# Kernel optimization log

Hardware: AMD Instinct MI355X
Metric: run time of the kernel (lower is better)

## Reference

```python
import jax, jax.numpy as jnp
import numpy as np

B_SZ, L_SEQ, D_MODEL, D_STATE = 4, 2048, 1024, 16


def setup_inputs() -> dict:
    key = jax.random.key(0)
    ks = jax.random.split(key, 6)
    x = jax.random.normal(ks[0], (B_SZ, L_SEQ, D_MODEL), jnp.float32)
    # HiPPO-inspired init: A_log = log(arange(1..n)).clamp(min=-7), broadcast over channels
    A_log = jnp.clip(jnp.log(jnp.arange(1, D_STATE + 1, dtype=jnp.float32)), -7.0, None)
    A_log = jnp.broadcast_to(A_log[None, :], (D_MODEL, D_STATE)).astype(jnp.float32)
    B_param = 0.02 * jax.random.normal(ks[1], (D_MODEL, D_STATE), jnp.float32)
    C_param = 0.02 * jax.random.normal(ks[2], (D_MODEL, D_STATE), jnp.float32)
    log_dt = 0.01 * jax.random.normal(ks[3], (D_MODEL,), jnp.float32) - 4.0
    in_w = jax.random.normal(ks[4], (2 * D_MODEL, D_MODEL), jnp.float32) / np.sqrt(D_MODEL).astype(np.float32)
    in_b = jnp.zeros((2 * D_MODEL,), jnp.float32)
    out_w = jax.random.normal(ks[5], (D_MODEL, D_MODEL), jnp.float32) / np.sqrt(D_MODEL).astype(np.float32)
    out_b = jnp.zeros((D_MODEL,), jnp.float32)
    ln_g = jnp.ones((D_MODEL,), jnp.float32)
    ln_b = jnp.zeros((D_MODEL,), jnp.float32)
    return {"x": x, "A_log": A_log, "B_param": B_param, "C_param": C_param,
            "log_dt": log_dt, "in_w": in_w, "in_b": in_b, "out_w": out_w,
            "out_b": out_b, "ln_g": ln_g, "ln_b": ln_b}


def _ssm_scan(u, A_log, B_param, C_param, log_dt):
    # u: (B, L, D). Builds kernel h[t,d] = sum_n A_bar[d,n]^t * C[d,n]*B[d,n]*dt[d]
    # and applies a causal depthwise convolution (via FFT; same math as conv1d).
    L = u.shape[1]
    dt = jnp.clip(jnp.exp(log_dt), 1e-4, 1.0)                      # (D,)
    A_bar = jnp.exp(-jnp.exp(A_log) * dt[:, None])                 # ZOH discretisation (D,N)
    A_bar = jnp.clip(A_bar, 1e-8, 1.0 - 1e-8)
    log_A = jnp.log(A_bar)                                         # (D,N)
    t_idx = jnp.arange(L, dtype=jnp.float32)                       # (L,)
    A_powers = jnp.exp(t_idx[:, None, None] * log_A[None, :, :])   # (L,D,N)
    cb_dt = C_param * B_param * dt[:, None]                        # (D,N)
    kernel = jnp.einsum('ldn,dn->ld', A_powers, cb_dt)             # (L,D)
    # causal conv: y[b,t,d] = sum_{tau<=t} kernel[tau,d] * u[b,t-tau,d]
    n_fft = 2 * L
    Kf = jnp.fft.rfft(kernel, n=n_fft, axis=0)                     # (n_fft/2+1, D)
    Uf = jnp.fft.rfft(u, n=n_fft, axis=1)                          # (B, n_fft/2+1, D)
    y = jnp.fft.irfft(Uf * Kf[None], n=n_fft, axis=1)[:, :L]       # (B,L,D)
    return y.astype(u.dtype)


def reference(x, A_log, B_param, C_param, log_dt, in_w, in_b, out_w, out_b, ln_g, ln_b):
    x = x.astype(jnp.float32)
    residual = x
    # LayerNorm (eps=1e-5)
    mu = jnp.mean(x, axis=-1, keepdims=True)
    var = jnp.mean(jnp.square(x - mu), axis=-1, keepdims=True)
    xn = (x - mu) * jax.lax.rsqrt(var + 1e-5) * ln_g + ln_b
    xz = xn @ in_w.T + in_b                                        # (B,L,2D)
    x_proj, z = xz[..., :D_MODEL], xz[..., D_MODEL:]
    z = jax.nn.silu(z)
    y = _ssm_scan(x_proj, A_log, B_param, C_param, log_dt)
    y = y * z
    y = y @ out_w.T + out_b
    # dropout is identity in eval mode
    return jnp.clip(y + residual, -10.0, 10.0)
```

## Files before the change

kernel.cpp:

```cpp
#include <hip/hip_runtime.h>
#include <hip/hip_bf16.h>

#define D_MODEL 1024
#define D_STATE 16
#define L_SEQ 2048
#define B_SZ 4
#define M_ROWS (B_SZ * L_SEQ)
#define N_CHUNK 32
#define C_LEN 64

typedef __attribute__((ext_vector_type(8))) short short8;
typedef __attribute__((ext_vector_type(4))) float f32x4;
typedef unsigned int u32;
typedef __attribute__((ext_vector_type(4))) u32 u32x4;

#define BAR() asm volatile("s_waitcnt lgkmcnt(0)\n\ts_barrier" ::: "memory")

static __device__ __forceinline__ unsigned short f2bf(float f) {
    unsigned int u = __float_as_uint(f);
    unsigned int r = (u + 0x7FFFu + ((u >> 16) & 1u)) >> 16;
    return (unsigned short)r;
}
static __device__ __forceinline__ float bf2f(unsigned short u) {
    return __uint_as_float(((unsigned int)u) << 16);
}

__global__ void conv_bf16_kernel(const float* __restrict__ src,
                                 unsigned short* __restrict__ dst, int n4) {
    int i = blockIdx.x * blockDim.x + threadIdx.x;
    if (i < n4) {
        float4 v = ((const float4*)src)[i];
        ushort4 o;
        o.x = f2bf(v.x); o.y = f2bf(v.y); o.z = f2bf(v.z); o.w = f2bf(v.w);
        ((ushort4*)dst)[i] = o;
    }
}

__global__ __launch_bounds__(256) void ln_kernel(const float* __restrict__ x,
                                                 const float* __restrict__ g,
                                                 const float* __restrict__ b,
                                                 unsigned short* __restrict__ xn) {
    int row = blockIdx.x;
    int t = threadIdx.x;
    const float4* xr = (const float4*)(x + (size_t)row * D_MODEL);
    float4 v = xr[t];
    float s  = v.x + v.y + v.z + v.w;
    float ss = v.x * v.x + v.y * v.y + v.z * v.z + v.w * v.w;
    #pragma unroll
    for (int o = 32; o > 0; o >>= 1) {
        s  += __shfl_down(s,  o);
        ss += __shfl_down(ss, o);
    }
    __shared__ float sbuf[8];
    int wid = t >> 6;
    if ((t & 63) == 0) { sbuf[wid] = s; sbuf[4 + wid] = ss; }
    __syncthreads();
    float S  = sbuf[0] + sbuf[1] + sbuf[2] + sbuf[3];
    float SS = sbuf[4] + sbuf[5] + sbuf[6] + sbuf[7];
    float mu  = S * (1.0f / D_MODEL);
    float var = SS * (1.0f / D_MODEL) - mu * mu;
    float inv = rsqrtf(var + 1e-5f);
    float4 gv = ((const float4*)g)[t];
    float4 bv = ((const float4*)b)[t];
    ushort4 o;
    o.x = f2bf((v.x - mu) * inv * gv.x + bv.x);
    o.y = f2bf((v.y - mu) * inv * gv.y + bv.y);
    o.z = f2bf((v.z - mu) * inv * gv.z + bv.z);
    o.w = f2bf((v.w - mu) * inv * gv.w + bv.w);
    ((ushort4*)(xn + (size_t)row * D_MODEL))[t] = o;
}

__global__ __launch_bounds__(256, 2) void gemm1_kernel(const unsigned short* __restrict__ A,
                                                       const unsigned short* __restrict__ Bt,
                                                       const float* __restrict__ bias,
                                                       unsigned short* __restrict__ u_bf,
                                                       unsigned short* __restrict__ zs) {
    __shared__ unsigned short lA[2][128 * 32];
    __shared__ unsigned short lB[2][256 * 32];
    const int K = D_MODEL;

    int t = threadIdx.x;
    int lane = t & 63;
    int wave = t >> 6;
    int wm = wave >> 1, wn = wave & 1;
    int m0 = blockIdx.x * 128;
    int n0 = blockIdx.y * 256;
    int row = lane & 15;
    int quad = lane >> 4;

    int sr = t >> 2;
    int sc = ((t & 3) ^ ((t >> 3) & 3)) * 8;
    const unsigned short* gA0 = A + (size_t)(m0 + sr) * K + sc;
    const unsigned short* gA1 = A + (size_t)(m0 + 64 + sr) * K + sc;
    const unsigned short* gB0 = Bt + (size_t)(n0 + sr) * K + sc;
    const unsigned short* gB1 = Bt + (size_t)(n0 + 64 + sr) * K + sc;
    const unsigned short* gB2 = Bt + (size_t)(n0 + 128 + sr) * K + sc;
    const unsigned short* gB3 = Bt + (size_t)(n0 + 192 + sr) * K + sc;

    int offA[4], offB[8];
    #pragma unroll
    for (int i = 0; i < 4; i++) {
        int r6 = i * 16 + row;
        int slot = r6 * 4 + (quad ^ ((r6 >> 1) & 3));
        offA[i] = wm * 2048 + slot * 8;
    }
    #pragma unroll
    for (int j = 0; j < 8; j++) {
        int r8 = wn * 128 + j * 16 + row;
        int half = r8 >> 6, r6 = r8 & 63;
        int slot = r6 * 4 + (quad ^ ((r6 >> 1) & 3));
        offB[j] = half * 2048 + slot * 8;
    }

    f32x4 acc[4][8] = {};

    u32x4 PA[6], PB[6];
    PA[0] = *(const u32x4*)gA0;        PA[1] = *(const u32x4*)gA1;
    PA[2] = *(const u32x4*)gB0;        PA[3] = *(const u32x4*)gB1;
    PA[4] = *(const u32x4*)gB2;        PA[5] = *(const u32x4*)gB3;
    PB[0] = *(const u32x4*)(gA0 + 32); PB[1] = *(const u32x4*)(gA1 + 32);
    PB[2] = *(const u32x4*)(gB0 + 32); PB[3] = *(const u32x4*)(gB1 + 32);
    PB[4] = *(const u32x4*)(gB2 + 32); PB[5] = *(const u32x4*)(gB3 + 32);

    for (int kk = 0; kk < K; kk += 64) {
        *(u32x4*)&lA[0][t * 8]        = PA[0];
        *(u32x4*)&lA[0][2048 + t * 8] = PA[1];
        *(u32x4*)&lB[0][t * 8]        = PA[2];
        *(u32x4*)&lB[0][2048 + t * 8] = PA[3];
        *(u32x4*)&lB[0][4096 + t * 8] = PA[4];
        *(u32x4*)&lB[0][6144 + t * 8] = PA[5];
        if (kk + 64 < K) {
            int kn = kk + 64;
            PA[0] = *(const u32x4*)(gA0 + kn); PA[1] = *(const u32x4*)(gA1 + kn);
            PA[2] = *(const u32x4*)(gB0 + kn); PA[3] = *(const u32x4*)(gB1 + kn);
            PA[4] = *(const u32x4*)(gB2 + kn); PA[5] = *(const u32x4*)(gB3 + kn);
        }
        BAR();
        {
            short8 a[4];
            #pragma unroll
            for (int i = 0; i < 4; i++) a[i] = *(const short8*)&lA[0][offA[i]];
            #pragma unroll
            for (int j = 0; j < 8; j++) {
                short8 b = *(const short8*)&lB[0][offB[j]];
                #pragma unroll
                for (int i = 0; i < 4; i++)
                    acc[i][j] = __builtin_amdgcn_mfma_f32_16x16x32_bf16(a[i], b, acc[i][j], 0, 0, 0);
            }
        }
        *(u32x4*)&lA[1][t * 8]        = PB[0];
        *(u32x4*)&lA[1][2048 + t * 8] = PB[1];
        *(u32x4*)&lB[1][t * 8]        = PB[2];
        *(u32x4*)&lB[1][2048 + t * 8] = PB[3];
        *(u32x4*)&lB[1][4096 + t * 8] = PB[4];
        *(u32x4*)&lB[1][6144 + t * 8] = PB[5];
        if (kk + 96 < K) {
            int kn = kk + 96;
            PB[0] = *(const u32x4*)(gA0 + kn); PB[1] = *(const u32x4*)(gA1 + kn);
            PB[2] = *(const u32x4*)(gB0 + kn); PB[3] = *(const u32x4*)(gB1 + kn);
            PB[4] = *(const u32x4*)(gB2 + kn); PB[5] = *(const u32x4*)(gB3 + kn);
        }
        BAR();
        {
            short8 a[4];
            #pragma unroll
            for (int i = 0; i < 4; i++) a[i] = *(const short8*)&lA[1][offA[i]];
            #pragma unroll
            for (int j = 0; j < 8; j++) {
                short8 b = *(const short8*)&lB[1][offB[j]];
                #pragma unroll
                for (int i = 0; i < 4; i++)
                    acc[i][j] = __builtin_amdgcn_mfma_f32_16x16x32_bf16(a[i], b, acc[i][j], 0, 0, 0);
            }
        }
    }

    int col = row;
    #pragma unroll
    for (int j = 0; j < 8; j++) {
        int n = n0 + wn * 128 + j * 16 + col;
        float bs = bias[n];
        #pragma unroll
        for (int i = 0; i < 4; i++) {
            #pragma unroll
            for (int r = 0; r < 4; r++) {
                int m = m0 + wm * 64 + i * 16 + quad * 4 + r;
                float v = acc[i][j][r] + bs;
                if (n < D_MODEL) {
                    u_bf[(size_t)m * D_MODEL + n] = f2bf(v);
                } else {
                    float sv = v / (1.0f + __expf(-v));
                    zs[(size_t)m * D_MODEL + (n - D_MODEL)] = f2bf(sv);
                }
            }
        }
    }
}

__global__ __launch_bounds__(256) void gemm2_kernel(const unsigned short* __restrict__ A,
                                                    const unsigned short* __restrict__ Bt,
                                                    const float* __restrict__ bias,
                                                    float* __restrict__ out_f,
                                                    const float* __restrict__ resid) {
    __shared__ unsigned short lA[2][128 * 32];
    __shared__ unsigned short lB[2][128 * 32];
    const int K = D_MODEL;

    int t = threadIdx.x;
    int lane = t & 63;
    int wave = t >> 6;
    int wm = wave >> 1, wn = wave & 1;
    int m0 = blockIdx.x * 128;
    int n0 = blockIdx.y * 128;
    int row = lane & 15;
    int quad = lane >> 4;

    int sr = t >> 2;
    int sc = ((t & 3) ^ ((t >> 3) & 3)) * 8;
    const unsigned short* gA0 = A + (size_t)(m0 + sr) * K + sc;
    const unsigned short* gA1 = A + (size_t)(m0 + 64 + sr) * K + sc;
    const unsigned short* gB0 = Bt + (size_t)(n0 + sr) * K + sc;
    const unsigned short* gB1 = Bt + (size_t)(n0 + 64 + sr) * K + sc;

    int offA[4], offB[4];
    #pragma unroll
    for (int i = 0; i < 4; i++) {
        int r6 = i * 16 + row;
        int slot = r6 * 4 + (quad ^ ((r6 >> 1) & 3));
        offA[i] = wm * 2048 + slot * 8;
        offB[i] = wn * 2048 + slot * 8;
    }

    f32x4 acc[4][4] = {};

    u32x4 PA[4], PB[4];
    PA[0] = *(const u32x4*)gA0;        PA[1] = *(const u32x4*)gA1;
    PA[2] = *(const u32x4*)gB0;        PA[3] = *(const u32x4*)gB1;
    PB[0] = *(const u32x4*)(gA0 + 32); PB[1] = *(const u32x4*)(gA1 + 32);
    PB[2] = *(const u32x4*)(gB0 + 32); PB[3] = *(const u32x4*)(gB1 + 32);

    for (int kk = 0; kk < K; kk += 64) {
        *(u32x4*)&lA[0][t * 8]        = PA[0];
        *(u32x4*)&lA[0][2048 + t * 8] = PA[1];
        *(u32x4*)&lB[0][t * 8]        = PA[2];
        *(u32x4*)&lB[0][2048 + t * 8] = PA[3];
        if (kk + 64 < K) {
            int kn = kk + 64;
            PA[0] = *(const u32x4*)(gA0 + kn); PA[1] = *(const u32x4*)(gA1 + kn);
            PA[2] = *(const u32x4*)(gB0 + kn); PA[3] = *(const u32x4*)(gB1 + kn);
        }
        BAR();
        {
            short8 a[4], b[4];
            #pragma unroll
            for (int i = 0; i < 4; i++) a[i] = *(const short8*)&lA[0][offA[i]];
            #pragma unroll
            for (int j = 0; j < 4; j++) b[j] = *(const short8*)&lB[0][offB[j]];
            #pragma unroll
            for (int i = 0; i < 4; i++)
                #pragma unroll
                for (int j = 0; j < 4; j++)
                    acc[i][j] = __builtin_amdgcn_mfma_f32_16x16x32_bf16(a[i], b[j], acc[i][j], 0, 0, 0);
        }
        *(u32x4*)&lA[1][t * 8]        = PB[0];
        *(u32x4*)&lA[1][2048 + t * 8] = PB[1];
        *(u32x4*)&lB[1][t * 8]        = PB[2];
        *(u32x4*)&lB[1][2048 + t * 8] = PB[3];
        if (kk + 96 < K) {
            int kn = kk + 96;
            PB[0] = *(const u32x4*)(gA0 + kn); PB[1] = *(const u32x4*)(gA1 + kn);
            PB[2] = *(const u32x4*)(gB0 + kn); PB[3] = *(const u32x4*)(gB1 + kn);
        }
        BAR();
        {
            short8 a[4], b[4];
            #pragma unroll
            for (int i = 0; i < 4; i++) a[i] = *(const short8*)&lA[1][offA[i]];
            #pragma unroll
            for (int j = 0; j < 4; j++) b[j] = *(const short8*)&lB[1][offB[j]];
            #pragma unroll
            for (int i = 0; i < 4; i++)
                #pragma unroll
                for (int j = 0; j < 4; j++)
                    acc[i][j] = __builtin_amdgcn_mfma_f32_16x16x32_bf16(a[i], b[j], acc[i][j], 0, 0, 0);
        }
    }

    int col = row;
    #pragma unroll
    for (int i = 0; i < 4; i++) {
        #pragma unroll
        for (int j = 0; j < 4; j++) {
            int n = n0 + wn * 64 + j * 16 + col;
            float bs = bias[n];
            #pragma unroll
            for (int r = 0; r < 4; r++) {
                int m = m0 + wm * 64 + i * 16 + quad * 4 + r;
                float y = acc[i][j][r] + bs + resid[(size_t)m * D_MODEL + n];
                y = fminf(10.0f, fmaxf(-10.0f, y));
                out_f[(size_t)m * D_MODEL + n] = y;
            }
        }
    }
}

static __device__ __forceinline__ void load_params(const float* __restrict__ A_log,
                                                   const float* __restrict__ log_dt,
                                                   int d, float* ab, float& dt_out) {
    float dt = fminf(1.0f, fmaxf(1e-4f, __expf(log_dt[d])));
    #pragma unroll
    for (int n = 0; n < D_STATE; n++) {
        float a = __expf(-__expf(A_log[d * D_STATE + n]) * dt);
        ab[n] = fminf(1.0f - 1e-8f, fmaxf(1e-8f, a));
    }
    dt_out = dt;
}

__global__ __launch_bounds__(256) void scan1_kernel(const unsigned short* __restrict__ u,
                                                    const float* __restrict__ A_log,
                                                    const float* __restrict__ log_dt,
                                                    float* __restrict__ s_local) {
    int gid = blockIdx.x * 256 + threadIdx.x;
    int d = gid & (D_MODEL - 1);
    int c = (gid >> 10) & (N_CHUNK - 1);
    int b = gid >> 15;

    float ab[D_STATE], dt;
    load_params(A_log, log_dt, d, ab, dt);

    float s[D_STATE];
    #pragma unroll
    for (int n = 0; n < D_STATE; n++) s[n] = 0.0f;

    const unsigned short* up = u + ((size_t)(b * L_SEQ + c * C_LEN)) * D_MODEL + d;
    for (int t = 0; t < C_LEN; t++) {
        float uv = bf2f(up[(size_t)t * D_MODEL]);
        #pragma unroll
        for (int n = 0; n < D_STATE; n++) s[n] = fmaf(ab[n], s[n], uv);
    }
    float* sl = s_local + ((size_t)(b * N_CHUNK + c) * D_STATE) * D_MODEL + d;
    #pragma unroll
    for (int n = 0; n < D_STATE; n++) sl[(size_t)n * D_MODEL] = s[n];
}

__global__ __launch_bounds__(256) void scan_combine_kernel(const float* __restrict__ s_local,
                                                           const float* __restrict__ A_log,
                                                           const float* __restrict__ log_dt,
                                                           float* __restrict__ s_init) {
    int gid = blockIdx.x * 256 + threadIdx.x;
    int d = gid & (D_MODEL - 1);
    int n = (gid >> 10) & (D_STATE - 1);
    int b = gid >> 14;

    float dt = fminf(1.0f, fmaxf(1e-4f, __expf(log_dt[d])));
    float a = __expf(-__expf(A_log[d * D_STATE + n]) * dt);
    a = fminf(1.0f - 1e-8f, fmaxf(1e-8f, a));
    float aP = a;
    #pragma unroll
    for (int q = 0; q < 6; q++) aP = aP * aP;

    float s = 0.0f;
    size_t stride_c = (size_t)D_STATE * D_MODEL;
    const float* sl = s_local + ((size_t)b * N_CHUNK * D_STATE + n) * D_MODEL + d;
    float* si = s_init + ((size_t)b * N_CHUNK * D_STATE + n) * D_MODEL + d;
    si[0] = 0.0f;
    for (int c = 1; c < N_CHUNK; c++) {
        s = fmaf(aP, s, sl[(size_t)(c - 1) * stride_c]);
        si[(size_t)c * stride_c] = s;
    }
}

__global__ __launch_bounds__(256) void scan2_kernel(const unsigned short* __restrict__ u,
                                                    const unsigned short* __restrict__ zs,
                                                    const float* __restrict__ A_log,
                                                    const float* __restrict__ Bp,
                                                    const float* __restrict__ Cp,
                                                    const float* __restrict__ log_dt,
                                                    const float* __restrict__ s_init,
                                                    unsigned short* __restrict__ yz) {
    int gid = blockIdx.x * 256 + threadIdx.x;
    int d = gid & (D_MODEL - 1);
    int c = (gid >> 10) & (N_CHUNK - 1);
    int b = gid >> 15;

    float ab[D_STATE], dt;
    load_params(A_log, log_dt, d, ab, dt);
    float cb[D_STATE];
    #pragma unroll
    for (int n = 0; n < D_STATE; n++)
        cb[n] = Cp[d * D_STATE + n] * Bp[d * D_STATE + n] * dt;

    float s[D_STATE];
    const float* si = s_init + ((size_t)(b * N_CHUNK + c) * D_STATE) * D_MODEL + d;
    #pragma unroll
    for (int n = 0; n < D_STATE; n++) s[n] = si[(size_t)n * D_MODEL];

    size_t m0 = (size_t)(b * L_SEQ + c * C_LEN);
    const unsigned short* up = u + m0 * D_MODEL + d;
    const unsigned short* zp = zs + m0 * D_MODEL + d;
    unsigned short* yp = yz + m0 * D_MODEL + d;

    for (int t = 0; t < C_LEN; t++) {
        float uv = bf2f(up[(size_t)t * D_MODEL]);
        #pragma unroll
        for (int n = 0; n < D_STATE; n++) s[n] = fmaf(ab[n], s[n], uv);
        float y = 0.0f;
        #pragma unroll
        for (int n = 0; n < D_STATE; n++) y = fmaf(cb[n], s[n], y);
        float zv = bf2f(zp[(size_t)t * D_MODEL]);
        yp[(size_t)t * D_MODEL] = f2bf(y * zv);
    }
}

extern "C" void kernel_launch(void* const* d_in, const int* in_sizes, int n_in,
                              void* d_out, int out_size, void* d_ws, size_t ws_size,
                              hipStream_t stream) {
    const float* x       = (const float*)d_in[0];
    const float* A_log   = (const float*)d_in[1];
    const float* B_param = (const float*)d_in[2];
    const float* C_param = (const float*)d_in[3];
    const float* log_dt  = (const float*)d_in[4];
    const float* in_w    = (const float*)d_in[5];
    const float* in_b    = (const float*)d_in[6];
    const float* out_w   = (const float*)d_in[7];
    const float* out_b   = (const float*)d_in[8];
    const float* ln_g    = (const float*)d_in[9];
    const float* ln_b    = (const float*)d_in[10];
    float* out = (float*)d_out;

    char* ws = (char*)d_ws;
    size_t off = 0;
    unsigned short* xn = (unsigned short*)(ws + off); off += (size_t)M_ROWS * D_MODEL * 2;
    unsigned short* w1 = (unsigned short*)(ws + off); off += (size_t)2 * D_MODEL * D_MODEL * 2;
    unsigned short* u  = (unsigned short*)(ws + off); off += (size_t)M_ROWS * D_MODEL * 2;
    unsigned short* zs = (unsigned short*)(ws + off); off += (size_t)M_ROWS * D_MODEL * 2;
    unsigned short* yz = (unsigned short*)(ws + off); off += (size_t)M_ROWS * D_MODEL * 2;
    unsigned short* w2 = (unsigned short*)(ws + off); off += (size_t)D_MODEL * D_MODEL * 2;
    float* s_local = (float*)(ws + off); off += (size_t)B_SZ * N_CHUNK * D_STATE * D_MODEL * 4;
    float* s_init  = (float*)(ws + off); off += (size_t)B_SZ * N_CHUNK * D_STATE * D_MODEL * 4;

    {
        int n4 = 2 * D_MODEL * D_MODEL / 4;
        conv_bf16_kernel<<<(n4 + 255) / 256, 256, 0, stream>>>(in_w, w1, n4);
    }
    {
        int n4 = D_MODEL * D_MODEL / 4;
        conv_bf16_kernel<<<(n4 + 255) / 256, 256, 0, stream>>>(out_w, w2, n4);
    }

    ln_kernel<<<M_ROWS, 256, 0, stream>>>(x, ln_g, ln_b, xn);

    gemm1_kernel<<<dim3(M_ROWS / 128, 2 * D_MODEL / 256), 256, 0, stream>>>(
        xn, w1, in_b, u, zs);

    scan1_kernel<<<(B_SZ * N_CHUNK * D_MODEL) / 256, 256, 0, stream>>>(u, A_log, log_dt, s_local);
    scan_combine_kernel<<<(B_SZ * D_STATE * D_MODEL) / 256, 256, 0, stream>>>(s_local, A_log, log_dt, s_init);
    scan2_kernel<<<(B_SZ * N_CHUNK * D_MODEL) / 256, 256, 0, stream>>>(
        u, zs, A_log, B_param, C_param, log_dt, s_init, yz);

    gemm2_kernel<<<dim3(M_ROWS / 128, D_MODEL / 128), 256, 0, stream>>>(
        yz, w2, out_b, out, x);
}
```

Before: 215.2 us.

## Rewrite both GEMMs with direct global-to-LDS loads and a 4-stage pipeline

Both projection GEMMs are rebuilt around direct global-to-LDS loads via global_load_lds, which removes the register staging step. A 4-slot LDS ring keeps three K-tiles in flight, gated by vmcnt waits and barriers. The blocks grow to 512 threads with larger tiles (256x256 for gemm1, 128x256 for gemm2), a swizzled block-to-tile mapping for L2 locality, and s_setprio raised around the MFMA bursts. This adds hand-managed wait counts and LDS swizzles that must match the loader lane mapping, and with 256 blocks the grid occupies the GPU in a single wave.

```diff
diff --git a/kernel.cpp b/kernel.cpp
--- a/kernel.cpp
+++ b/kernel.cpp
@@ -11,10 +11,15 @@
 
 typedef __attribute__((ext_vector_type(8))) short short8;
 typedef __attribute__((ext_vector_type(4))) float f32x4;
-typedef unsigned int u32;
-typedef __attribute__((ext_vector_type(4))) u32 u32x4;
-
-#define BAR() asm volatile("s_waitcnt lgkmcnt(0)\n\ts_barrier" ::: "memory")
+
+#define SBAR()  asm volatile("s_barrier" ::: "memory")
+#define GATE(N) asm volatile("s_waitcnt vmcnt(" #N ") lgkmcnt(0)\n\ts_barrier" ::: "memory")
+
+typedef const unsigned short __attribute__((address_space(1))) gas_us;
+typedef unsigned short __attribute__((address_space(3))) las_us;
+static __device__ __forceinline__ void gload16(const unsigned short* g, unsigned short* l) {
+    __builtin_amdgcn_global_load_lds((gas_us*)g, (las_us*)l, 16, 0, 0);
+}
 
 static __device__ __forceinline__ unsigned short f2bf(float f) {
     unsigned int u = __float_as_uint(f);
@@ -70,123 +75,99 @@
     ((ushort4*)(xn + (size_t)row * D_MODEL))[t] = o;
 }
 
-__global__ __launch_bounds__(256, 2) void gemm1_kernel(const unsigned short* __restrict__ A,
+#define MFMA16(ACC, I0, AV, BV) { \
+    _Pragma("unroll") for (int i_ = 0; i_ < 4; ++i_) { \
+        _Pragma("unroll") for (int jf_ = 0; jf_ < 4; ++jf_) \
+            ACC[(I0) + i_][jf_] = __builtin_amdgcn_mfma_f32_16x16x32_bf16( \
+                AV[i_], BV[jf_], ACC[(I0) + i_][jf_], 0, 0, 0); } }
+
+#define STAGE1A(J) { size_t ko_ = (size_t)(J) * 32; int so_ = ((J) & 3) * 16384; \
+    gload16(pA0 + ko_, dA0 + so_); gload16(pA1 + ko_, dA1 + so_); }
+#define STAGE1B(J) { size_t ko_ = (size_t)(J) * 32; int so_ = ((J) & 3) * 16384; \
+    gload16(pB0 + ko_, dB0 + so_); gload16(pB1 + ko_, dB1 + so_); }
+
+#define G1_TILE(J, DOSTAGE, TRAIL) { \
+    const int slot_ = (J) & 3; \
+    const char* rA_ = ldsA_rd + slot_ * 32768; \
+    const char* rB_ = ldsB_rd + slot_ * 32768; \
+    short8 av[4], bv[4]; \
+    _Pragma("unroll") for (int j_ = 0; j_ < 4; ++j_) bv[j_] = *(const short8*)(rB_ + j_ * 1024); \
+    _Pragma("unroll") for (int i_ = 0; i_ < 4; ++i_) av[i_] = *(const short8*)(rA_ + i_ * 1024); \
+    if (DOSTAGE) { STAGE1A((J) + 3); } \
+    SBAR(); \
+    __builtin_amdgcn_s_setprio(1); \
+    MFMA16(acc, 0, av, bv); \
+    __builtin_amdgcn_s_setprio(0); \
+    SBAR(); \
+    _Pragma("unroll") for (int i_ = 0; i_ < 4; ++i_) av[i_] = *(const short8*)(rA_ + 4096 + i_ * 1024); \
+    if (DOSTAGE) { STAGE1B((J) + 3); } \
+    SBAR(); \
+    __builtin_amdgcn_s_setprio(1); \
+    MFMA16(acc, 4, av, bv); \
+    __builtin_amdgcn_s_setprio(0); \
+    TRAIL; \
+}
+
+__global__ __launch_bounds__(512, 2) void gemm1_kernel(const unsigned short* __restrict__ A,
                                                        const unsigned short* __restrict__ Bt,
                                                        const float* __restrict__ bias,
                                                        unsigned short* __restrict__ u_bf,
                                                        unsigned short* __restrict__ zs) {
-    __shared__ unsigned short lA[2][128 * 32];
-    __shared__ unsigned short lB[2][256 * 32];
+    __shared__ __align__(16) unsigned short lds[4][2][8192];
     const int K = D_MODEL;
 
     int t = threadIdx.x;
     int lane = t & 63;
     int wave = t >> 6;
-    int wm = wave >> 1, wn = wave & 1;
-    int m0 = blockIdx.x * 128;
-    int n0 = blockIdx.y * 256;
-    int row = lane & 15;
+    int wm = wave >> 2;
+    int wn = wave & 3;
+
+    int bid = blockIdx.x;
+    int swz = (bid & 7) * 32 + (bid >> 3);
+    int m0 = (swz >> 3) * 256;
+    int n0 = (swz & 7) * 256;
+
+    int srow = lane >> 2;
+    int sk = ((lane & 3) * 8) ^ ((lane & 32) >> 1);
+    const unsigned short* pA0 = A  + (size_t)(m0 + wave * 16 + srow) * K + sk;
+    const unsigned short* pA1 = pA0 + (size_t)128 * K;
+    const unsigned short* pB0 = Bt + (size_t)(n0 + wave * 16 + srow) * K + sk;
+    const unsigned short* pB1 = pB0 + (size_t)128 * K;
+
+    unsigned short* dA0 = &lds[0][0][wave * 512];
+    unsigned short* dA1 = &lds[0][0][(8 + wave) * 512];
+    unsigned short* dB0 = &lds[0][1][wave * 512];
+    unsigned short* dB1 = &lds[0][1][(8 + wave) * 512];
+
+    int off_base = (lane & 15) * 64 + (((lane >> 4) * 16) ^ ((lane & 8) * 4));
+    const char* ldsA_rd = (const char*)(&lds[0][0][0]) + wm * 8192 + off_base;
+    const char* ldsB_rd = (const char*)(&lds[0][1][0]) + wn * 4096 + off_base;
+
+    f32x4 acc[8][4] = {};
+
+    STAGE1A(0); STAGE1B(0); STAGE1A(1); STAGE1B(1); STAGE1A(2); STAGE1B(2);
+    GATE(8);
+
+    #pragma unroll 1
+    for (int j = 0; j < 29; ++j) { G1_TILE(j, true, GATE(8)); }
+    G1_TILE(29, false, GATE(4));
+    G1_TILE(30, false, GATE(0));
+    G1_TILE(31, false, (void)0);
+
+    int col = lane & 15;
     int quad = lane >> 4;
-
-    int sr = t >> 2;
-    int sc = ((t & 3) ^ ((t >> 3) & 3)) * 8;
-    const unsigned short* gA0 = A + (size_t)(m0 + sr) * K + sc;
-    const unsigned short* gA1 = A + (size_t)(m0 + 64 + sr) * K + sc;
-    const unsigned short* gB0 = Bt + (size_t)(n0 + sr) * K + sc;
-    const unsigned short* gB1 = Bt + (size_t)(n0 + 64 + sr) * K + sc;
-    const unsigned short* gB2 = Bt + (size_t)(n0 + 128 + sr) * K + sc;
-    const unsigned short* gB3 = Bt + (size_t)(n0 + 192 + sr) * K + sc;
-
-    int offA[4], offB[8];
-    #pragma unroll
-    for (int i = 0; i < 4; i++) {
-        int r6 = i * 16 + row;
-        int slot = r6 * 4 + (quad ^ ((r6 >> 1) & 3));
-        offA[i] = wm * 2048 + slot * 8;
-    }
-    #pragma unroll
-    for (int j = 0; j < 8; j++) {
-        int r8 = wn * 128 + j * 16 + row;
-        int half = r8 >> 6, r6 = r8 & 63;
-        int slot = r6 * 4 + (quad ^ ((r6 >> 1) & 3));
-        offB[j] = half * 2048 + slot * 8;
-    }
-
-    f32x4 acc[4][8] = {};
-
-    u32x4 PA[6], PB[6];
-    PA[0] = *(const u32x4*)gA0;        PA[1] = *(const u32x4*)gA1;
-    PA[2] = *(const u32x4*)gB0;        PA[3] = *(const u32x4*)gB1;
-    PA[4] = *(const u32x4*)gB2;        PA[5] = *(const u32x4*)gB3;
-    PB[0] = *(const u32x4*)(gA0 + 32); PB[1] = *(const u32x4*)(gA1 + 32);
-    PB[2] = *(const u32x4*)(gB0 + 32); PB[3] = *(const u32x4*)(gB1 + 32);
-    PB[4] = *(const u32x4*)(gB2 + 32); PB[5] = *(const u32x4*)(gB3 + 32);
-
-    for (int kk = 0; kk < K; kk += 64) {
-        *(u32x4*)&lA[0][t * 8]        = PA[0];
-        *(u32x4*)&lA[0][2048 + t * 8] = PA[1];
-        *(u32x4*)&lB[0][t * 8]        = PA[2];
-        *(u32x4*)&lB[0][2048 + t * 8] = PA[3];
-        *(u32x4*)&lB[0][4096 + t * 8] = PA[4];
-        *(u32x4*)&lB[0][6144 + t * 8] = PA[5];
-        if (kk + 64 < K) {
-            int kn = kk + 64;
-            PA[0] = *(const u32x4*)(gA0 + kn); PA[1] = *(const u32x4*)(gA1 + kn);
-            PA[2] = *(const u32x4*)(gB0 + kn); PA[3] = *(const u32x4*)(gB1 + kn);
-            PA[4] = *(const u32x4*)(gB2 + kn); PA[5] = *(const u32x4*)(gB3 + kn);
-        }
-        BAR();
-        {
-            short8 a[4];
+    #pragma unroll
+    for (int jf = 0; jf < 4; ++jf) {
+        int n = n0 + wn * 64 + jf * 16 + col;
+        float bs = bias[n];
+        bool isU = (n < D_MODEL);
+        #pragma unroll
+        for (int i = 0; i < 8; ++i) {
             #pragma unroll
-            for (int i = 0; i < 4; i++) a[i] = *(const short8*)&lA[0][offA[i]];
-            #pragma unroll
-            for (int j = 0; j < 8; j++) {
-                short8 b = *(const short8*)&lB[0][offB[j]];
-                #pragma unroll
-                for (int i = 0; i < 4; i++)
-                    acc[i][j] = __builtin_amdgcn_mfma_f32_16x16x32_bf16(a[i], b, acc[i][j], 0, 0, 0);
-            }
-        }
-        *(u32x4*)&lA[1][t * 8]        = PB[0];
-        *(u32x4*)&lA[1][2048 + t * 8] = PB[1];
-        *(u32x4*)&lB[1][t * 8]        = PB[2];
-        *(u32x4*)&lB[1][2048 + t * 8] = PB[3];
-        *(u32x4*)&lB[1][4096 + t * 8] = PB[4];
-        *(u32x4*)&lB[1][6144 + t * 8] = PB[5];
-        if (kk + 96 < K) {
-            int kn = kk + 96;
-            PB[0] = *(const u32x4*)(gA0 + kn); PB[1] = *(const u32x4*)(gA1 + kn);
-            PB[2] = *(const u32x4*)(gB0 + kn); PB[3] = *(const u32x4*)(gB1 + kn);
-            PB[4] = *(const u32x4*)(gB2 + kn); PB[5] = *(const u32x4*)(gB3 + kn);
-        }
-        BAR();
-        {
-            short8 a[4];
-            #pragma unroll
-            for (int i = 0; i < 4; i++) a[i] = *(const short8*)&lA[1][offA[i]];
-            #pragma unroll
-            for (int j = 0; j < 8; j++) {
-                short8 b = *(const short8*)&lB[1][offB[j]];
-                #pragma unroll
-                for (int i = 0; i < 4; i++)
-                    acc[i][j] = __builtin_amdgcn_mfma_f32_16x16x32_bf16(a[i], b, acc[i][j], 0, 0, 0);
-            }
-        }
-    }
-
-    int col = row;
-    #pragma unroll
-    for (int j = 0; j < 8; j++) {
-        int n = n0 + wn * 128 + j * 16 + col;
-        float bs = bias[n];
-        #pragma unroll
-        for (int i = 0; i < 4; i++) {
-            #pragma unroll
-            for (int r = 0; r < 4; r++) {
-                int m = m0 + wm * 64 + i * 16 + quad * 4 + r;
-                float v = acc[i][j][r] + bs;
-                if (n < D_MODEL) {
+            for (int r = 0; r < 4; ++r) {
+                int m = m0 + wm * 128 + i * 16 + quad * 4 + r;
+                float v = acc[i][jf][r] + bs;
+                if (isU) {
                     u_bf[(size_t)m * D_MODEL + n] = f2bf(v);
                 } else {
                     float sv = v / (1.0f + __expf(-v));
@@ -197,106 +178,80 @@
     }
 }
 
-__global__ __launch_bounds__(256) void gemm2_kernel(const unsigned short* __restrict__ A,
-                                                    const unsigned short* __restrict__ Bt,
-                                                    const float* __restrict__ bias,
-                                                    float* __restrict__ out_f,
-                                                    const float* __restrict__ resid) {
-    __shared__ unsigned short lA[2][128 * 32];
-    __shared__ unsigned short lB[2][128 * 32];
+#define STAGE2(J) { size_t ko_ = (size_t)(J) * 32; int so_ = ((J) & 3) * 12288; \
+    gload16(pA0 + ko_, dA + so_); gload16(pB0 + ko_, dB0 + so_); gload16(pB1 + ko_, dB1 + so_); }
+
+#define G2_TILE(J, DOSTAGE, TRAIL) { \
+    const int slot_ = (J) & 3; \
+    const char* rA_ = ldsA_rd + slot_ * 24576; \
+    const char* rB_ = ldsB_rd + slot_ * 24576; \
+    short8 av[4], bv[4]; \
+    _Pragma("unroll") for (int i_ = 0; i_ < 4; ++i_) av[i_] = *(const short8*)(rA_ + i_ * 1024); \
+    _Pragma("unroll") for (int j_ = 0; j_ < 4; ++j_) bv[j_] = *(const short8*)(rB_ + j_ * 1024); \
+    if (DOSTAGE) { STAGE2((J) + 3); } \
+    SBAR(); \
+    __builtin_amdgcn_s_setprio(1); \
+    MFMA16(acc, 0, av, bv); \
+    __builtin_amdgcn_s_setprio(0); \
+    TRAIL; \
+}
+
+__global__ __launch_bounds__(512, 2) void gemm2_kernel(const unsigned short* __restrict__ A,
+                                                       const unsigned short* __restrict__ Bt,
+                                                       const float* __restrict__ bias,
+                                                       float* __restrict__ out_f,
+                                                       const float* __restrict__ resid) {
+    __shared__ __align__(16) unsigned short lds[4][12288];
     const int K = D_MODEL;
 
     int t = threadIdx.x;
     int lane = t & 63;
     int wave = t >> 6;
-    int wm = wave >> 1, wn = wave & 1;
-    int m0 = blockIdx.x * 128;
-    int n0 = blockIdx.y * 128;
-    int row = lane & 15;
+    int wm = wave >> 2;
+    int wn = wave & 3;
+
+    int bid = blockIdx.x;
+    int swz = (bid & 7) * 32 + (bid >> 3);
+    int m0 = (swz >> 2) * 128;
+    int n0 = (swz & 3) * 256;
+
+    int srow = lane >> 2;
+    int sk = ((lane & 3) * 8) ^ ((lane & 32) >> 1);
+    const unsigned short* pA0 = A  + (size_t)(m0 + wave * 16 + srow) * K + sk;
+    const unsigned short* pB0 = Bt + (size_t)(n0 + wave * 16 + srow) * K + sk;
+    const unsigned short* pB1 = pB0 + (size_t)128 * K;
+
+    unsigned short* dA  = &lds[0][wave * 512];
+    unsigned short* dB0 = &lds[0][4096 + wave * 512];
+    unsigned short* dB1 = &lds[0][8192 + wave * 512];
+
+    int off_base = (lane & 15) * 64 + (((lane >> 4) * 16) ^ ((lane & 8) * 4));
+    const char* ldsA_rd = (const char*)(&lds[0][0]) + wm * 4096 + off_base;
+    const char* ldsB_rd = (const char*)(&lds[0][0]) + 8192 + wn * 4096 + off_base;
+
+    f32x4 acc[4][4] = {};
+
+    STAGE2(0); STAGE2(1); STAGE2(2);
+    GATE(6);
+
+    #pragma unroll 1
+    for (int j = 0; j < 29; ++j) { G2_TILE(j, true, GATE(6)); }
+    G2_TILE(29, false, GATE(3));
+    G2_TILE(30, false, GATE(0));
+    G2_TILE(31, false, (void)0);
+
+    int col = lane & 15;
     int quad = lane >> 4;
-
-    int sr = t >> 2;
-    int sc = ((t & 3) ^ ((t >> 3) & 3)) * 8;
-    const unsigned short* gA0 = A + (size_t)(m0 + sr) * K + sc;
-    const unsigned short* gA1 = A + (size_t)(m0 + 64 + sr) * K + sc;
-    const unsigned short* gB0 = Bt + (size_t)(n0 + sr) * K + sc;
-    const unsigned short* gB1 = Bt + (size_t)(n0 + 64 + sr) * K + sc;
-
-    int offA[4], offB[4];
-    #pragma unroll
-    for (int i = 0; i < 4; i++) {
-        int r6 = i * 16 + row;
-        int slot = r6 * 4 + (quad ^ ((r6 >> 1) & 3));
-        offA[i] = wm * 2048 + slot * 8;
-        offB[i] = wn * 2048 + slot * 8;
-    }
-
-    f32x4 acc[4][4] = {};
-
-    u32x4 PA[4], PB[4];
-    PA[0] = *(const u32x4*)gA0;        PA[1] = *(const u32x4*)gA1;
-    PA[2] = *(const u32x4*)gB0;        PA[3] = *(const u32x4*)gB1;
-    PB[0] = *(const u32x4*)(gA0 + 32); PB[1] = *(const u32x4*)(gA1 + 32);
-    PB[2] = *(const u32x4*)(gB0 + 32); PB[3] = *(const u32x4*)(gB1 + 32);
-
-    for (int kk = 0; kk < K; kk += 64) {
-        *(u32x4*)&lA[0][t * 8]        = PA[0];
-        *(u32x4*)&lA[0][2048 + t * 8] = PA[1];
-        *(u32x4*)&lB[0][t * 8]        = PA[2];
-        *(u32x4*)&lB[0][2048 + t * 8] = PA[3];
-        if (kk + 64 < K) {
-            int kn = kk + 64;
-            PA[0] = *(const u32x4*)(gA0 + kn); PA[1] = *(const u32x4*)(gA1 + kn);
-            PA[2] = *(const u32x4*)(gB0 + kn); PA[3] = *(const u32x4*)(gB1 + kn);
-        }
-        BAR();
-        {
-            short8 a[4], b[4];
+    #pragma unroll
+    for (int jf = 0; jf < 4; ++jf) {
+        int n = n0 + wn * 64 + jf * 16 + col;
+        float bs = bias[n];
+        #pragma unroll
+        for (int i = 0; i < 4; ++i) {
             #pragma unroll
-            for (int i = 0; i < 4; i++) a[i] = *(const short8*)&lA[0][offA[i]];
-            #pragma unroll
-            for (int j = 0; j < 4; j++) b[j] = *(const short8*)&lB[0][offB[j]];
-            #pragma unroll
-            for (int i = 0; i < 4; i++)
-                #pragma unroll
-                for (int j = 0; j < 4; j++)
-                    acc[i][j] = __builtin_amdgcn_mfma_f32_16x16x32_bf16(a[i], b[j], acc[i][j], 0, 0, 0);
-        }
-        *(u32x4*)&lA[1][t * 8]        = PB[0];
-        *(u32x4*)&lA[1][2048 + t * 8] = PB[1];
-        *(u32x4*)&lB[1][t * 8]        = PB[2];
-        *(u32x4*)&lB[1][2048 + t * 8] = PB[3];
-        if (kk + 96 < K) {
-            int kn = kk + 96;
-            PB[0] = *(const u32x4*)(gA0 + kn); PB[1] = *(const u32x4*)(gA1 + kn);
-            PB[2] = *(const u32x4*)(gB0 + kn); PB[3] = *(const u32x4*)(gB1 + kn);
-        }
-        BAR();
-        {
-            short8 a[4], b[4];
-            #pragma unroll
-            for (int i = 0; i < 4; i++) a[i] = *(const short8*)&lA[1][offA[i]];
-            #pragma unroll
-            for (int j = 0; j < 4; j++) b[j] = *(const short8*)&lB[1][offB[j]];
-            #pragma unroll
-            for (int i = 0; i < 4; i++)
-                #pragma unroll
-                for (int j = 0; j < 4; j++)
-                    acc[i][j] = __builtin_amdgcn_mfma_f32_16x16x32_bf16(a[i], b[j], acc[i][j], 0, 0, 0);
-        }
-    }
-
-    int col = row;
-    #pragma unroll
-    for (int i = 0; i < 4; i++) {
-        #pragma unroll
-        for (int j = 0; j < 4; j++) {
-            int n = n0 + wn * 64 + j * 16 + col;
-            float bs = bias[n];
-            #pragma unroll
-            for (int r = 0; r < 4; r++) {
+            for (int r = 0; r < 4; ++r) {
                 int m = m0 + wm * 64 + i * 16 + quad * 4 + r;
-                float y = acc[i][j][r] + bs + resid[(size_t)m * D_MODEL + n];
+                float y = acc[i][jf][r] + bs + resid[(size_t)m * D_MODEL + n];
                 y = fminf(10.0f, fmaxf(-10.0f, y));
                 out_f[(size_t)m * D_MODEL + n] = y;
             }
@@ -450,14 +405,12 @@
 
     ln_kernel<<<M_ROWS, 256, 0, stream>>>(x, ln_g, ln_b, xn);
 
-    gemm1_kernel<<<dim3(M_ROWS / 128, 2 * D_MODEL / 256), 256, 0, stream>>>(
-        xn, w1, in_b, u, zs);
+    gemm1_kernel<<<256, 512, 0, stream>>>(xn, w1, in_b, u, zs);
 
     scan1_kernel<<<(B_SZ * N_CHUNK * D_MODEL) / 256, 256, 0, stream>>>(u, A_log, log_dt, s_local);
     scan_combine_kernel<<<(B_SZ * D_STATE * D_MODEL) / 256, 256, 0, stream>>>(s_local, A_log, log_dt, s_init);
     scan2_kernel<<<(B_SZ * N_CHUNK * D_MODEL) / 256, 256, 0, stream>>>(
         u, zs, A_log, B_param, C_param, log_dt, s_init, yz);
 
-    gemm2_kernel<<<dim3(M_ROWS / 128, D_MODEL / 128), 256, 0, stream>>>(
-        yz, w2, out_b, out, x);
-}
+    gemm2_kernel<<<256, 512, 0, stream>>>(yz, w2, out_b, out, x);
+}
```

Result: no change. 214.3 us (-0.4%).
